# Optimization experiments

Measured on AMD Instinct MI355X. Metric: run time of the kernel, lower is better.

## Reference

```python
import jax, jax.numpy as jnp
import numpy as np

N, DX, DZ, DY, H = 8192, 64, 128, 16, 512


def setup_inputs() -> dict:
    key = jax.random.key(0)
    ks = jax.random.split(key, 8)
    s1 = 1.0 / np.sqrt(DX)
    s2 = 1.0 / np.sqrt(H)
    return {
        "z_pred": jax.random.normal(ks[0], (N, DZ), dtype=jnp.float32),
        "x_label": jax.random.normal(ks[1], (N, DX), dtype=jnp.float32),
        "y_label": jax.random.normal(ks[2], (N, DY), dtype=jnp.float32),
        "W1": jax.random.normal(ks[3], (DX, H), dtype=jnp.float32) * s1,
        "b1": jnp.zeros((H,), dtype=jnp.float32),
        "W2": jax.random.normal(ks[4], (H, DZ), dtype=jnp.float32) * s2,
        "b2": jnp.zeros((DZ,), dtype=jnp.float32),
        "A": jax.random.normal(ks[5], (DZ, DZ), dtype=jnp.float32) * (1.0 / np.sqrt(DZ)),
        "B": jax.random.normal(ks[6], (DZ, DY), dtype=jnp.float32) * (1.0 / np.sqrt(DY)),
    }


def reference(z_pred, x_label, y_label, W1, b1, W2, b2, A, B):
    # forward_mapper T: x (dx,) -> (dz,), 2-layer tanh MLP
    def T(x):
        return jnp.tanh(x @ W1 + b1) @ W2 + b2

    # diff_eq: per-sample nonlinear dynamics x_dot = tanh(x)
    x_dot = jnp.tanh(x_label)  # (N, dx)

    # per-sample Jacobian dT/dx: (N, dz, dx). Equivalent to the torch code's
    # full N x N batched Jacobian followed by the diagonal slice, but without
    # the O(N^2) waste.
    jac = jax.vmap(jax.jacrev(T))(x_label)  # (N, dz, dx)

    dtdx_mul_f = jnp.einsum("nzd,nd->nz", jac, x_dot)  # (N, dz)
    m_mul_t = z_pred @ A.T                              # (N, dz)
    k_mul_h = y_label @ B.T                             # (N, dz)

    pde = dtdx_mul_f - m_mul_t - k_mul_h                # (N, dz)
    loss_batch = jnp.linalg.norm(pde, axis=1)           # (N,)
    return jnp.mean(loss_batch)
```

## Files before the change

kernel.cpp:

```cpp
#include <hip/hip_runtime.h>
#include <math.h>

#define Nn   8192
#define DXc  64
#define DZc  128
#define DYc  16
#define Hc   512
#define NKC  21

typedef short bf16x8 __attribute__((ext_vector_type(8)));
typedef float f32x4  __attribute__((ext_vector_type(4)));

__device__ __forceinline__ float fast_tanh(float x) {
    float e = __expf(2.0f * x);
    return 1.0f - 2.0f / (e + 1.0f);
}
__device__ __forceinline__ short f2bf(float f) {
    unsigned u = __float_as_uint(f);
    return (short)((u + 0x7FFFu + ((u >> 16) & 1u)) >> 16);
}
__device__ __forceinline__ bf16x8 pack8(float4 a, float4 b) {
    bf16x8 r;
    r[0]=f2bf(a.x); r[1]=f2bf(a.y); r[2]=f2bf(a.z); r[3]=f2bf(a.w);
    r[4]=f2bf(b.x); r[5]=f2bf(b.y); r[6]=f2bf(b.z); r[7]=f2bf(b.w);
    return r;
}

__global__ __launch_bounds__(256)
void prep_kernel(const float* __restrict__ W1,
                 const float* __restrict__ W2,
                 const float* __restrict__ A,
                 const float* __restrict__ Bm,
                 short* __restrict__ Wb,
                 short* __restrict__ Wf,
                 float* __restrict__ out) {
    int c = blockIdx.x * 256 + threadIdx.x;
    if (c == 0) out[0] = 0.f;

    if (c < 4096) {
        int lane = c & 63, block = c >> 6;
        int n16 = lane & 15, q = lane >> 4;
        int j = (block >> 1) * 16 + n16;
        int k0 = (block & 1) * 32 + q * 8;
        bf16x8 v;
#pragma unroll
        for (int i = 0; i < 8; i++) v[i] = f2bf(W1[(size_t)(k0 + i) * Hc + j]);
        *(bf16x8*)(Wb + (size_t)c * 8) = v;
    } else {
        int c2 = c - 4096;
        int lane = c2 & 63, block = c2 >> 6;
        int zt = block / 21, kc = block % 21;
        int n16 = lane & 15, q = lane >> 4;
        int z = zt * 16 + n16;
        bf16x8 v = (bf16x8){0,0,0,0,0,0,0,0};
        if (kc < 16) {
            int k0 = kc * 32 + q * 8;
#pragma unroll
            for (int i = 0; i < 8; i++) v[i] = f2bf(W2[(size_t)(k0 + i) * DZc + z]);
        } else if (kc < 20) {
            int c0 = (kc - 16) * 32 + q * 8;
            float4 a0 = *(const float4*)(A + (size_t)z * DZc + c0);
            float4 a1 = *(const float4*)(A + (size_t)z * DZc + c0 + 4);
            v[0]=f2bf(-a0.x); v[1]=f2bf(-a0.y); v[2]=f2bf(-a0.z); v[3]=f2bf(-a0.w);
            v[4]=f2bf(-a1.x); v[5]=f2bf(-a1.y); v[6]=f2bf(-a1.z); v[7]=f2bf(-a1.w);
        } else if (q < 2) {
            float4 b0 = *(const float4*)(Bm + (size_t)z * DYc + q * 8);
            float4 b1 = *(const float4*)(Bm + (size_t)z * DYc + q * 8 + 4);
            v[0]=f2bf(-b0.x); v[1]=f2bf(-b0.y); v[2]=f2bf(-b0.z); v[3]=f2bf(-b0.w);
            v[4]=f2bf(-b1.x); v[5]=f2bf(-b1.y); v[6]=f2bf(-b1.z); v[7]=f2bf(-b1.w);
        }
        *(bf16x8*)(Wf + (size_t)c2 * 8) = v;
    }
}

#define MFMA16(a, b, c) __builtin_amdgcn_mfma_f32_16x16x32_bf16((a), (b), (c), 0, 0, 0)

__global__ __launch_bounds__(256, 4)
void pde_main(const float* __restrict__ z_pred,
              const float* __restrict__ x_label,
              const float* __restrict__ y_label,
              const float* __restrict__ b1,
              const short* __restrict__ Wb,
              const short* __restrict__ Wf,
              float* __restrict__ out) {
    __shared__ __align__(16) short sS[16 * 512];
    __shared__ float red[4][16];

    const int tid  = threadIdx.x;
    const int w    = tid >> 6;
    const int lane = tid & 63;
    const int n16  = lane & 15;
    const int q    = lane >> 4;
    const int n0   = blockIdx.x * 16;

    const float* xp = x_label + (size_t)(n0 + n16) * DXc + q * 8;
    float4 x0 = *(const float4*)xp,        x1 = *(const float4*)(xp + 4);
    float4 x2 = *(const float4*)(xp + 32), x3 = *(const float4*)(xp + 36);
    bf16x8 ax0 = pack8(x0, x1), ax1 = pack8(x2, x3);
    bf16x8 at0, at1;
    {
        float v[16] = {x0.x,x0.y,x0.z,x0.w, x1.x,x1.y,x1.z,x1.w,
                       x2.x,x2.y,x2.z,x2.w, x3.x,x3.y,x3.z,x3.w};
#pragma unroll
        for (int i = 0; i < 8; i++) { at0[i] = f2bf(fast_tanh(v[i])); at1[i] = f2bf(fast_tanh(v[8 + i])); }
    }

#pragma unroll
    for (int t = 0; t < 8; t++) {
        const int jt = 8 * w + t;
        const short* bp = Wb + (size_t)(jt * 2 * 64 + lane) * 8;
        bf16x8 bw0 = *(const bf16x8*)bp;
        bf16x8 bw1 = *(const bf16x8*)(bp + 512);
        f32x4 h = (f32x4){0.f,0.f,0.f,0.f};
        f32x4 u = (f32x4){0.f,0.f,0.f,0.f};
        h = MFMA16(ax0, bw0, h);  h = MFMA16(ax1, bw1, h);
        u = MFMA16(at0, bw0, u);  u = MFMA16(at1, bw1, u);
        const float bj = b1[jt * 16 + n16];
        const int j = jt * 16 + n16;
        const int sbase = (j >> 5) * 512 + ((j >> 3) & 3) * 128 + (j & 7);
#pragma unroll
        for (int reg = 0; reg < 4; reg++) {
            float tv = fast_tanh(h[reg] + bj);
            float s  = (1.f - tv * tv) * u[reg];
            sS[sbase + (q * 4 + reg) * 8] = f2bf(s);
        }
    }

    const short* wf0 = Wf + (size_t)((2 * w)     * NKC * 64 + lane) * 8;
    const short* wf1 = Wf + (size_t)((2 * w + 1) * NKC * 64 + lane) * 8;
    f32x4 acc0 = (f32x4){0.f,0.f,0.f,0.f};
    f32x4 acc1 = (f32x4){0.f,0.f,0.f,0.f};
    {
        const float* zp = z_pred + (size_t)(n0 + n16) * DZc + q * 8;
#pragma unroll
        for (int kcl = 0; kcl < 4; kcl++) {
            float4 a0 = *(const float4*)(zp + kcl * 32);
            float4 a1 = *(const float4*)(zp + kcl * 32 + 4);
            bf16x8 az = pack8(a0, a1);
            acc0 = MFMA16(az, *(const bf16x8*)(wf0 + (16 + kcl) * 512), acc0);
            acc1 = MFMA16(az, *(const bf16x8*)(wf1 + (16 + kcl) * 512), acc1);
        }
        bf16x8 ay = (bf16x8){0,0,0,0,0,0,0,0};
        if (q < 2) {
            const float* yp = y_label + (size_t)(n0 + n16) * DYc + q * 8;
            ay = pack8(*(const float4*)yp, *(const float4*)(yp + 4));
        }
        acc0 = MFMA16(ay, *(const bf16x8*)(wf0 + 20 * 512), acc0);
        acc1 = MFMA16(ay, *(const bf16x8*)(wf1 + 20 * 512), acc1);
    }

    __syncthreads();

#pragma unroll
    for (int kc = 0; kc < 16; kc++) {
        bf16x8 sa = *(const bf16x8*)(sS + kc * 512 + lane * 8);
        acc0 = MFMA16(sa, *(const bf16x8*)(wf0 + kc * 512), acc0);
        acc1 = MFMA16(sa, *(const bf16x8*)(wf1 + kc * 512), acc1);
    }

#pragma unroll
    for (int reg = 0; reg < 4; reg++) {
        float sq = fmaf(acc0[reg], acc0[reg], acc1[reg] * acc1[reg]);
        sq += __shfl_xor(sq, 1);
        sq += __shfl_xor(sq, 2);
        sq += __shfl_xor(sq, 4);
        sq += __shfl_xor(sq, 8);
        if (n16 == 0) red[w][q * 4 + reg] = sq;
    }
    __syncthreads();

    if (tid < 16) {
        float tot = red[0][tid] + red[1][tid] + red[2][tid] + red[3][tid];
        float nrm = sqrtf(tot);
        nrm += __shfl_xor(nrm, 1);
        nrm += __shfl_xor(nrm, 2);
        nrm += __shfl_xor(nrm, 4);
        nrm += __shfl_xor(nrm, 8);
        if (tid == 0) atomicAdd(out, nrm * (1.0f / (float)Nn));
    }
}

extern "C" void kernel_launch(void* const* d_in, const int* in_sizes, int n_in,
                              void* d_out, int out_size, void* d_ws, size_t ws_size,
                              hipStream_t stream) {
    const float* z_pred  = (const float*)d_in[0];
    const float* x_label = (const float*)d_in[1];
    const float* y_label = (const float*)d_in[2];
    const float* W1      = (const float*)d_in[3];
    const float* b1      = (const float*)d_in[4];
    const float* W2      = (const float*)d_in[5];
    const float* A       = (const float*)d_in[7];
    const float* Bm      = (const float*)d_in[8];

    short* Wb = (short*)d_ws;
    short* Wf = Wb + 512 * DXc;

    prep_kernel<<<58, 256, 0, stream>>>(W1, W2, A, Bm, Wb, Wf, (float*)d_out);
    pde_main<<<Nn / 16, 256, 0, stream>>>(z_pred, x_label, y_label, b1, Wb, Wf, (float*)d_out);
}
```

Measured before the change: 86.75 us.

## Process 32 samples per 512-thread block to reuse weight fragments

Each block now handles two 16-sample groups with 8 waves instead of one group with 4 waves, so every loaded W1/W2/A/B bf16 fragment feeds two MFMAs (one per group). Each wave now owns one 16-column output tile instead of two, and the hidden-layer tiles are split across 8 waves. The aim is to halve global/L2 weight traffic per sample and the number of blocks and atomics. The cost is twice the LDS use per block, fewer blocks in the grid (256), and possibly lower occupancy.

```diff
diff --git a/kernel.cpp b/kernel.cpp
--- a/kernel.cpp
+++ b/kernel.cpp
@@ -75,7 +75,7 @@
 
 #define MFMA16(a, b, c) __builtin_amdgcn_mfma_f32_16x16x32_bf16((a), (b), (c), 0, 0, 0)
 
-__global__ __launch_bounds__(256, 4)
+__global__ __launch_bounds__(512, 2)
 void pde_main(const float* __restrict__ z_pred,
               const float* __restrict__ x_label,
               const float* __restrict__ y_label,
@@ -83,99 +83,114 @@
               const short* __restrict__ Wb,
               const short* __restrict__ Wf,
               float* __restrict__ out) {
-    __shared__ __align__(16) short sS[16 * 512];
-    __shared__ float red[4][16];
+    __shared__ __align__(16) short sS[2][16 * 512];
+    __shared__ float red[8][2][16];
 
     const int tid  = threadIdx.x;
     const int w    = tid >> 6;
     const int lane = tid & 63;
     const int n16  = lane & 15;
     const int q    = lane >> 4;
-    const int n0   = blockIdx.x * 16;
-
-    const float* xp = x_label + (size_t)(n0 + n16) * DXc + q * 8;
-    float4 x0 = *(const float4*)xp,        x1 = *(const float4*)(xp + 4);
-    float4 x2 = *(const float4*)(xp + 32), x3 = *(const float4*)(xp + 36);
-    bf16x8 ax0 = pack8(x0, x1), ax1 = pack8(x2, x3);
-    bf16x8 at0, at1;
-    {
+    const int n0   = blockIdx.x * 32;
+
+    bf16x8 ax0[2], ax1[2], at0[2], at1[2];
+#pragma unroll
+    for (int g = 0; g < 2; g++) {
+        const float* xp = x_label + (size_t)(n0 + g * 16 + n16) * DXc + q * 8;
+        float4 x0 = *(const float4*)xp,        x1 = *(const float4*)(xp + 4);
+        float4 x2 = *(const float4*)(xp + 32), x3 = *(const float4*)(xp + 36);
+        ax0[g] = pack8(x0, x1);  ax1[g] = pack8(x2, x3);
         float v[16] = {x0.x,x0.y,x0.z,x0.w, x1.x,x1.y,x1.z,x1.w,
                        x2.x,x2.y,x2.z,x2.w, x3.x,x3.y,x3.z,x3.w};
 #pragma unroll
-        for (int i = 0; i < 8; i++) { at0[i] = f2bf(fast_tanh(v[i])); at1[i] = f2bf(fast_tanh(v[8 + i])); }
-    }
-
-#pragma unroll
-    for (int t = 0; t < 8; t++) {
-        const int jt = 8 * w + t;
+        for (int i = 0; i < 8; i++) { at0[g][i] = f2bf(fast_tanh(v[i])); at1[g][i] = f2bf(fast_tanh(v[8 + i])); }
+    }
+
+#pragma unroll
+    for (int t = 0; t < 4; t++) {
+        const int jt = 4 * w + t;
         const short* bp = Wb + (size_t)(jt * 2 * 64 + lane) * 8;
         bf16x8 bw0 = *(const bf16x8*)bp;
         bf16x8 bw1 = *(const bf16x8*)(bp + 512);
-        f32x4 h = (f32x4){0.f,0.f,0.f,0.f};
-        f32x4 u = (f32x4){0.f,0.f,0.f,0.f};
-        h = MFMA16(ax0, bw0, h);  h = MFMA16(ax1, bw1, h);
-        u = MFMA16(at0, bw0, u);  u = MFMA16(at1, bw1, u);
         const float bj = b1[jt * 16 + n16];
         const int j = jt * 16 + n16;
         const int sbase = (j >> 5) * 512 + ((j >> 3) & 3) * 128 + (j & 7);
 #pragma unroll
+        for (int g = 0; g < 2; g++) {
+            f32x4 h = (f32x4){0.f,0.f,0.f,0.f};
+            f32x4 u = (f32x4){0.f,0.f,0.f,0.f};
+            h = MFMA16(ax0[g], bw0, h);  h = MFMA16(ax1[g], bw1, h);
+            u = MFMA16(at0[g], bw0, u);  u = MFMA16(at1[g], bw1, u);
+#pragma unroll
+            for (int reg = 0; reg < 4; reg++) {
+                float tv = fast_tanh(h[reg] + bj);
+                float s  = (1.f - tv * tv) * u[reg];
+                sS[g][sbase + (q * 4 + reg) * 8] = f2bf(s);
+            }
+        }
+    }
+
+    const short* wfb = Wf + (size_t)(w * NKC * 64 + lane) * 8;
+    f32x4 acc[2] = {(f32x4){0.f,0.f,0.f,0.f}, (f32x4){0.f,0.f,0.f,0.f}};
+    {
+#pragma unroll
+        for (int kcl = 0; kcl < 4; kcl++) {
+            bf16x8 bz = *(const bf16x8*)(wfb + (16 + kcl) * 512);
+#pragma unroll
+            for (int g = 0; g < 2; g++) {
+                const float* zp = z_pred + (size_t)(n0 + g * 16 + n16) * DZc + kcl * 32 + q * 8;
+                bf16x8 az = pack8(*(const float4*)zp, *(const float4*)(zp + 4));
+                acc[g] = MFMA16(az, bz, acc[g]);
+            }
+        }
+        bf16x8 by = *(const bf16x8*)(wfb + 20 * 512);
+#pragma unroll
+        for (int g = 0; g < 2; g++) {
+            bf16x8 ay = (bf16x8){0,0,0,0,0,0,0,0};
+            if (q < 2) {
+                const float* yp = y_label + (size_t)(n0 + g * 16 + n16) * DYc + q * 8;
+                ay = pack8(*(const float4*)yp, *(const float4*)(yp + 4));
+            }
+            acc[g] = MFMA16(ay, by, acc[g]);
+        }
+    }
+
+    __syncthreads();
+
+#pragma unroll
+    for (int kc = 0; kc < 16; kc++) {
+        bf16x8 bk = *(const bf16x8*)(wfb + kc * 512);
+        bf16x8 sa0 = *(const bf16x8*)(sS[0] + kc * 512 + lane * 8);
+        bf16x8 sa1 = *(const bf16x8*)(sS[1] + kc * 512 + lane * 8);
+        acc[0] = MFMA16(sa0, bk, acc[0]);
+        acc[1] = MFMA16(sa1, bk, acc[1]);
+    }
+
+#pragma unroll
+    for (int g = 0; g < 2; g++) {
+#pragma unroll
         for (int reg = 0; reg < 4; reg++) {
-            float tv = fast_tanh(h[reg] + bj);
-            float s  = (1.f - tv * tv) * u[reg];
-            sS[sbase + (q * 4 + reg) * 8] = f2bf(s);
-        }
-    }
-
-    const short* wf0 = Wf + (size_t)((2 * w)     * NKC * 64 + lane) * 8;
-    const short* wf1 = Wf + (size_t)((2 * w + 1) * NKC * 64 + lane) * 8;
-    f32x4 acc0 = (f32x4){0.f,0.f,0.f,0.f};
-    f32x4 acc1 = (f32x4){0.f,0.f,0.f,0.f};
-    {
-        const float* zp = z_pred + (size_t)(n0 + n16) * DZc + q * 8;
-#pragma unroll
-        for (int kcl = 0; kcl < 4; kcl++) {
-            float4 a0 = *(const float4*)(zp + kcl * 32);
-            float4 a1 = *(const float4*)(zp + kcl * 32 + 4);
-            bf16x8 az = pack8(a0, a1);
-            acc0 = MFMA16(az, *(const bf16x8*)(wf0 + (16 + kcl) * 512), acc0);
-            acc1 = MFMA16(az, *(const bf16x8*)(wf1 + (16 + kcl) * 512), acc1);
-        }
-        bf16x8 ay = (bf16x8){0,0,0,0,0,0,0,0};
-        if (q < 2) {
-            const float* yp = y_label + (size_t)(n0 + n16) * DYc + q * 8;
-            ay = pack8(*(const float4*)yp, *(const float4*)(yp + 4));
-        }
-        acc0 = MFMA16(ay, *(const bf16x8*)(wf0 + 20 * 512), acc0);
-        acc1 = MFMA16(ay, *(const bf16x8*)(wf1 + 20 * 512), acc1);
-    }
-
+            float sq = acc[g][reg] * acc[g][reg];
+            sq += __shfl_xor(sq, 1);
+            sq += __shfl_xor(sq, 2);
+            sq += __shfl_xor(sq, 4);
+            sq += __shfl_xor(sq, 8);
+            if (n16 == 0) red[w][g][q * 4 + reg] = sq;
+        }
+    }
     __syncthreads();
 
-#pragma unroll
-    for (int kc = 0; kc < 16; kc++) {
-        bf16x8 sa = *(const bf16x8*)(sS + kc * 512 + lane * 8);
-        acc0 = MFMA16(sa, *(const bf16x8*)(wf0 + kc * 512), acc0);
-        acc1 = MFMA16(sa, *(const bf16x8*)(wf1 + kc * 512), acc1);
-    }
-
-#pragma unroll
-    for (int reg = 0; reg < 4; reg++) {
-        float sq = fmaf(acc0[reg], acc0[reg], acc1[reg] * acc1[reg]);
-        sq += __shfl_xor(sq, 1);
-        sq += __shfl_xor(sq, 2);
-        sq += __shfl_xor(sq, 4);
-        sq += __shfl_xor(sq, 8);
-        if (n16 == 0) red[w][q * 4 + reg] = sq;
-    }
-    __syncthreads();
-
-    if (tid < 16) {
-        float tot = red[0][tid] + red[1][tid] + red[2][tid] + red[3][tid];
+    if (tid < 32) {
+        const int g = tid >> 4, r = tid & 15;
+        float tot = 0.f;
+#pragma unroll
+        for (int i = 0; i < 8; i++) tot += red[i][g][r];
         float nrm = sqrtf(tot);
         nrm += __shfl_xor(nrm, 1);
         nrm += __shfl_xor(nrm, 2);
         nrm += __shfl_xor(nrm, 4);
         nrm += __shfl_xor(nrm, 8);
+        nrm += __shfl_xor(nrm, 16);
         if (tid == 0) atomicAdd(out, nrm * (1.0f / (float)Nn));
     }
 }
@@ -196,5 +211,5 @@
     short* Wf = Wb + 512 * DXc;
 
     prep_kernel<<<58, 256, 0, stream>>>(W1, W2, A, Bm, Wb, Wf, (float*)d_out);
-    pde_main<<<Nn / 16, 256, 0, stream>>>(z_pred, x_label, y_label, b1, Wb, Wf, (float*)d_out);
-}
+    pde_main<<<Nn / 32, 512, 0, stream>>>(z_pred, x_label, y_label, b1, Wb, Wf, (float*)d_out);
+}
```

Result: no change. 86.28 us (-0.5%).
